# Performance work log

Measured on AMD Instinct MI355X. Metric: run time of the kernel, lower is better.

Reference implementation:

```python
import jax, jax.numpy as jnp
import numpy as np

N = 100_000      # nodes
E = 3_200_000    # edges (avg degree 32)
HID = 64         # hid_dim == in_dim
T = 4            # S2V propagation rounds


def setup_inputs() -> dict:
    key = jax.random.key(0)
    ks = jax.random.split(key, 10)
    s = lambda fan: 1.0 / np.sqrt(fan)
    return {
        "x": jax.random.normal(ks[0], (N, HID), jnp.float32),
        "x_tag": jax.random.uniform(ks[1], (N,), jnp.float32),
        "edge_attr": jax.random.uniform(ks[2], (E, 1), jnp.float32),
        "edge_index": jax.random.randint(ks[3], (2, E), 0, N, dtype=jnp.int32),
        # per-layer bias-free Linear weights (stored as [in, out])
        "W1": jax.random.normal(ks[4], (T, HID), jnp.float32),            # lin1: 1 -> hid
        "W2": jax.random.normal(ks[5], (T, HID, HID), jnp.float32) * s(HID),  # lin2: in -> hid
        "W4": jax.random.normal(ks[6], (T, HID), jnp.float32),            # lin4: 1 -> hid
        "W5": jax.random.normal(ks[7], (2 * HID, 1), jnp.float32) * s(2 * HID),  # lin5
        "W6": jax.random.normal(ks[8], (HID, HID), jnp.float32) * s(HID),  # lin6
        "W7": jax.random.normal(ks[9], (HID, HID), jnp.float32) * s(HID),  # lin7
    }


def reference(x, x_tag, edge_attr, edge_index, W1, W2, W4, W5, W6, W7):
    src = edge_index[0]  # j (message source / p3 scatter target)
    dst = edge_index[1]  # i (aggregation target)
    for l in range(T):  # fixed small layer count
        p1 = x_tag[:, None] * W1[l][None, :]                        # lin1(x_tag)  [N,HID]
        e = jax.nn.relu(edge_attr * W4[l][None, :])                  # relu(lin4(edge_attr)) [E,HID]
        aggr = jax.ops.segment_sum(x[src], dst, num_segments=N)     # add-aggregate x_j at i
        p2 = aggr @ W2[l]                                            # lin2(aggr_out)
        p3 = jax.ops.segment_sum(e, src, num_segments=N)             # scatter_add at edge_index[0]
        x = jax.nn.relu(p1 + p2 + p3)
    graph_pool = jnp.sum(x, axis=0, keepdims=True) @ W6              # [1,HID]
    nodes_vec = x @ W7                                               # [N,HID]
    cat = jnp.concatenate(
        [jnp.broadcast_to(graph_pool, (x.shape[0], graph_pool.shape[1])), nodes_vec], axis=1
    )
    Q = jax.nn.relu(cat) @ W5                                        # [N,1]
    return Q
```

## Files before the change

kernel.cpp:

```cpp
#include <hip/hip_runtime.h>

constexpr int NN  = 100000;
constexpr int NE  = 3200000;
constexpr int HID = 64;
constexpr int TL  = 4;

constexpr int BIN_SHIFT = 9;
constexpr int BIN_NODES = 1 << BIN_SHIFT;
constexpr int NBINS     = (NN + BIN_NODES - 1) / BIN_NODES;
constexpr int BINCAP    = 18944;
constexpr int TILE_E    = 2048;

typedef unsigned short ushort_t;
typedef unsigned int uint_t;
typedef __attribute__((ext_vector_type(8))) short bf16x8;
typedef __attribute__((ext_vector_type(4))) float f32x4;

__device__ __forceinline__ ushort_t f2b(float f) {
  uint_t u = __float_as_uint(f);
  u += 0x7fff + ((u >> 16) & 1);
  return (ushort_t)(u >> 16);
}
__device__ __forceinline__ float b2f(ushort_t h) {
  return __uint_as_float(((uint_t)h) << 16);
}

__global__ __launch_bounds__(256) void escatter_kernel(
    const int* __restrict__ ei, const float* __restrict__ ea,
    int* __restrict__ bincursor, uint_t* __restrict__ gbin,
    int* __restrict__ bincursor2, uint_t* __restrict__ gbin2) {
  __shared__ int hist1[NBINS], base1[NBINS];
  __shared__ int hist2[NBINS], base2[NBINS];
  int tid = threadIdx.x;
  int ntiles = (NE + TILE_E - 1) / TILE_E;
  for (int tile = blockIdx.x; tile < ntiles; tile += gridDim.x) {
    int tb = tile * TILE_E;
    for (int i = tid; i < NBINS; i += 256) { hist1[i] = 0; hist2[i] = 0; }
    __syncthreads();
    uint_t rec1[8], rec2[8]; int bn1[8], bn2[8], rk1[8], rk2[8];
    #pragma unroll
    for (int j = 0; j < 8; ++j) {
      int e = tb + tid + j * 256;
      bn1[j] = -1; bn2[j] = -1;
      rk1[j] = 0; rk2[j] = 0; rec1[j] = 0; rec2[j] = 0;
      if (e < NE) {
        int s = ei[e];
        int d = ei[NE + e];
        uint_t q = (uint_t)(int)(ea[e] * 8388608.0f);
        bn1[j] = d >> BIN_SHIFT;
        rec1[j] = ((uint_t)s << BIN_SHIFT) | (uint_t)(d & (BIN_NODES - 1));
        rk1[j] = atomicAdd(&hist1[bn1[j]], 1);
        bn2[j] = s >> BIN_SHIFT;
        rec2[j] = (q << BIN_SHIFT) | (uint_t)(s & (BIN_NODES - 1));
        rk2[j] = atomicAdd(&hist2[bn2[j]], 1);
      }
    }
    __syncthreads();
    for (int i = tid; i < NBINS; i += 256) {
      int c1 = hist1[i];
      base1[i] = c1 ? atomicAdd(&bincursor[i], c1) : 0;
      int c2 = hist2[i];
      base2[i] = c2 ? atomicAdd(&bincursor2[i], c2) : 0;
    }
    __syncthreads();
    #pragma unroll
    for (int j = 0; j < 8; ++j) {
      if (bn1[j] >= 0) {
        int p1 = base1[bn1[j]] + rk1[j];
        if (p1 < BINCAP) gbin[(size_t)bn1[j] * BINCAP + p1] = rec1[j];
        int p2 = base2[bn2[j]] + rk2[j];
        if (p2 < BINCAP) gbin2[(size_t)bn2[j] * BINCAP + p2] = rec2[j];
      }
    }
    __syncthreads();
  }
}

__global__ __launch_bounds__(256) void binscatter_kernel(
    const int* __restrict__ ei, int* __restrict__ bincursor,
    uint_t* __restrict__ gbin) {
  __shared__ int hist[NBINS];
  __shared__ int base[NBINS];
  int tid = threadIdx.x;
  int ntiles = (NE + TILE_E - 1) / TILE_E;
  for (int tile = blockIdx.x; tile < ntiles; tile += gridDim.x) {
    int tb = tile * TILE_E;
    for (int i = tid; i < NBINS; i += 256) hist[i] = 0;
    __syncthreads();
    uint_t rec[8]; int bn[8]; int rk[8];
    #pragma unroll
    for (int j = 0; j < 8; ++j) {
      int e = tb + tid + j * 256;
      bn[j] = -1; rk[j] = 0; rec[j] = 0;
      if (e < NE) {
        int s = ei[e];
        int d = ei[NE + e];
        bn[j] = d >> BIN_SHIFT;
        rec[j] = ((uint_t)s << BIN_SHIFT) | (uint_t)(d & (BIN_NODES - 1));
        rk[j] = atomicAdd(&hist[bn[j]], 1);
      }
    }
    __syncthreads();
    for (int i = tid; i < NBINS; i += 256) {
      int c = hist[i];
      base[i] = c ? atomicAdd(&bincursor[i], c) : 0;
    }
    __syncthreads();
    #pragma unroll
    for (int j = 0; j < 8; ++j) {
      if (bn[j] >= 0) {
        int pos = base[bn[j]] + rk[j];
        if (pos < BINCAP) gbin[(size_t)bn[j] * BINCAP + pos] = rec[j];
      }
    }
    __syncthreads();
  }
}

__global__ __launch_bounds__(256) void sbinscatter_kernel(
    const int* __restrict__ ei, const float* __restrict__ ea,
    int* __restrict__ bincursor2, uint_t* __restrict__ gbin) {
  __shared__ int hist[NBINS];
  __shared__ int base[NBINS];
  int tid = threadIdx.x;
  int ntiles = (NE + TILE_E - 1) / TILE_E;
  for (int tile = blockIdx.x; tile < ntiles; tile += gridDim.x) {
    int tb = tile * TILE_E;
    for (int i = tid; i < NBINS; i += 256) hist[i] = 0;
    __syncthreads();
    uint_t rec[8]; int bn[8]; int rk[8];
    #pragma unroll
    for (int j = 0; j < 8; ++j) {
      int e = tb + tid + j * 256;
      bn[j] = -1; rk[j] = 0; rec[j] = 0;
      if (e < NE) {
        int s = ei[e];
        uint_t q = (uint_t)(int)(ea[e] * 8388608.0f);
        bn[j] = s >> BIN_SHIFT;
        rec[j] = (q << BIN_SHIFT) | (uint_t)(s & (BIN_NODES - 1));
        rk[j] = atomicAdd(&hist[bn[j]], 1);
      }
    }
    __syncthreads();
    for (int i = tid; i < NBINS; i += 256) {
      int c = hist[i];
      base[i] = c ? atomicAdd(&bincursor2[i], c) : 0;
    }
    __syncthreads();
    #pragma unroll
    for (int j = 0; j < 8; ++j) {
      if (bn[j] >= 0) {
        int pos = base[bn[j]] + rk[j];
        if (pos < BINCAP) gbin[(size_t)bn[j] * BINCAP + pos] = rec[j];
      }
    }
    __syncthreads();
  }
}

__global__ __launch_bounds__(256) void bucket_kernel(
    const uint_t* __restrict__ gbin, const int* __restrict__ bincursor,
    int* __restrict__ colidx, int* __restrict__ cnt, int cap) {
  __shared__ int cur[BIN_NODES];
  int b = blockIdx.x;
  int tid = threadIdx.x;
  for (int i = tid; i < BIN_NODES; i += 256) cur[i] = 0;
  __syncthreads();
  int cb = min(bincursor[b], BINCAP);
  const uint_t* g = gbin + (size_t)b * BINCAP;
  for (int i = tid; i < cb; i += 256) {
    uint_t r = g[i];
    int dl = (int)(r & (BIN_NODES - 1));
    int src = (int)(r >> BIN_SHIFT);
    int pos = atomicAdd(&cur[dl], 1);
    int n = (b << BIN_SHIFT) + dl;
    if (pos < cap) colidx[(size_t)n * cap + pos] = src;
  }
  __syncthreads();
  for (int i = tid; i < BIN_NODES; i += 256) {
    int n = (b << BIN_SHIFT) + i;
    if (n < NN) cnt[n] = min(cur[i], cap);
  }
  for (int gsl = tid; gsl < BIN_NODES * 64; gsl += 256) {
    int i = gsl >> 6;
    int s = gsl & 63;
    int n = (b << BIN_SHIFT) + i;
    if (n < NN && s < 48 && s >= cur[i]) colidx[(size_t)n * cap + s] = NN;
  }
}

__global__ __launch_bounds__(256) void s3bucket_kernel(
    const uint_t* __restrict__ gbin, const int* __restrict__ bincursor2,
    int* __restrict__ s3i) {
  __shared__ int acc[BIN_NODES];
  int b = blockIdx.x;
  int tid = threadIdx.x;
  for (int i = tid; i < BIN_NODES; i += 256) acc[i] = 0;
  __syncthreads();
  int cb = min(bincursor2[b], BINCAP);
  const uint_t* g = gbin + (size_t)b * BINCAP;
  for (int i = tid; i < cb; i += 256) {
    uint_t r = g[i];
    atomicAdd(&acc[r & (BIN_NODES - 1)], (int)(r >> BIN_SHIFT));
  }
  __syncthreads();
  for (int i = tid; i < BIN_NODES; i += 256) {
    int n = (b << BIN_SHIFT) + i;
    if (n < NN) s3i[n] = acc[i];
  }
}

__global__ void conv_kernel(const float* __restrict__ x, ushort_t* __restrict__ xb) {
  int i = blockIdx.x * blockDim.x + threadIdx.x;
  if (i * 4 >= NN * HID) return;
  const float4 v = *reinterpret_cast<const float4*>(&x[i * 4]);
  ushort4 o;
  o.x = f2b(v.x); o.y = f2b(v.y); o.z = f2b(v.z); o.w = f2b(v.w);
  *reinterpret_cast<ushort4*>(&xb[i * 4]) = o;
}

__global__ void wconv_kernel(const float* __restrict__ W2,
                             const float* __restrict__ W7,
                             ushort_t* __restrict__ w2t,
                             ushort_t* __restrict__ w7t) {
  int i = blockIdx.x * blockDim.x + threadIdx.x;
  int tot2 = TL * HID * HID;
  if (i < tot2) {
    int l = i >> 12, r = i & 4095, h = r >> 6, k = r & 63;
    w2t[i] = f2b(W2[(size_t)l * 4096 + k * 64 + h]);
  } else if (i < tot2 + HID * HID) {
    int j = i - tot2, h = j >> 6, k = j & 63;
    w7t[j] = f2b(W7[k * 64 + h]);
  }
}

__global__ __launch_bounds__(256) void dense_kernel(
    const ushort_t* __restrict__ xin, const ushort_t* __restrict__ wt,
    ushort_t* __restrict__ yout) {
  int lane = threadIdx.x & 63;
  int wv = (blockIdx.x * blockDim.x + threadIdx.x) >> 6;
  int n0 = wv * 32;
  if (n0 >= NN) return;
  int row = lane & 15;
  int ks = (lane >> 4) * 8;
  bf16x8 a0 = *(const bf16x8*)&xin[(size_t)(n0 + row) * HID + ks];
  bf16x8 a1 = *(const bf16x8*)&xin[(size_t)(n0 + row) * HID + 32 + ks];
  bf16x8 a2 = *(const bf16x8*)&xin[(size_t)(n0 + 16 + row) * HID + ks];
  bf16x8 a3 = *(const bf16x8*)&xin[(size_t)(n0 + 16 + row) * HID + 32 + ks];
  #pragma unroll
  for (int ct = 0; ct < 4; ++ct) {
    bf16x8 b0 = *(const bf16x8*)&wt[(ct * 16 + row) * HID + ks];
    bf16x8 b1 = *(const bf16x8*)&wt[(ct * 16 + row) * HID + 32 + ks];
    f32x4 acc0 = {0.f, 0.f, 0.f, 0.f};
    f32x4 acc1 = {0.f, 0.f, 0.f, 0.f};
    acc0 = __builtin_amdgcn_mfma_f32_16x16x32_bf16(a0, b0, acc0, 0, 0, 0);
    acc0 = __builtin_amdgcn_mfma_f32_16x16x32_bf16(a1, b1, acc0, 0, 0, 0);
    acc1 = __builtin_amdgcn_mfma_f32_16x16x32_bf16(a2, b0, acc1, 0, 0, 0);
    acc1 = __builtin_amdgcn_mfma_f32_16x16x32_bf16(a3, b1, acc1, 0, 0, 0);
    int rr = (lane >> 4) * 4;
    #pragma unroll
    for (int r = 0; r < 4; ++r) {
      yout[(size_t)(n0 + rr + r) * HID + ct * 16 + row] = f2b(acc0[r]);
      yout[(size_t)(n0 + 16 + rr + r) * HID + ct * 16 + row] = f2b(acc1[r]);
    }
  }
}

__global__ __launch_bounds__(256) void aggr_kernel(
    const ushort_t* __restrict__ yin, ushort_t* __restrict__ xout,
    const int* __restrict__ cnt, const int* __restrict__ colidx, int cap,
    const float* __restrict__ x_tag, const int* __restrict__ s3i,
    const float* __restrict__ W1l, const float* __restrict__ W4l) {
  int lane = threadIdx.x & 63;
  int wv = (blockIdx.x * blockDim.x + threadIdx.x) >> 6;
  int n0 = wv * 2;
  if (n0 >= NN) return;
  int half = lane >> 5;
  int n = n0 + half;
  int grp = (lane >> 3) & 3;
  int sub = lane & 7;
  const int* cl = colidx + (size_t)n * cap + grp;
  float f0 = 0.f, f1 = 0.f, f2 = 0.f, f3 = 0.f;
  float f4 = 0.f, f5 = 0.f, f6 = 0.f, f7 = 0.f;
  uint4 w[12];
  #pragma unroll
  for (int j = 0; j < 12; ++j) {
    int c = cl[j * 4];
    w[j] = *reinterpret_cast<const uint4*>(&yin[(size_t)c * HID + sub * 8]);
  }
  #pragma unroll
  for (int j = 0; j < 12; ++j) {
    f0 += __uint_as_float(w[j].x << 16);
    f1 += __uint_as_float(w[j].x & 0xffff0000u);
    f2 += __uint_as_float(w[j].y << 16);
    f3 += __uint_as_float(w[j].y & 0xffff0000u);
    f4 += __uint_as_float(w[j].z << 16);
    f5 += __uint_as_float(w[j].z & 0xffff0000u);
    f6 += __uint_as_float(w[j].w << 16);
    f7 += __uint_as_float(w[j].w & 0xffff0000u);
  }
  int deg = cnt[n];
  if (__any(deg > 48)) {
    int t2 = deg - 48;
    const int* ct2 = colidx + (size_t)n * cap + 48;
    for (int jt = 0; jt < 12; ++jt) {
      int idx = jt * 4 + grp;
      if (idx < t2) {
        int c = ct2[idx];
        uint4 ww = *reinterpret_cast<const uint4*>(&yin[(size_t)c * HID + sub * 8]);
        f0 += __uint_as_float(ww.x << 16);
        f1 += __uint_as_float(ww.x & 0xffff0000u);
        f2 += __uint_as_float(ww.y << 16);
        f3 += __uint_as_float(ww.y & 0xffff0000u);
        f4 += __uint_as_float(ww.z << 16);
        f5 += __uint_as_float(ww.z & 0xffff0000u);
        f6 += __uint_as_float(ww.w << 16);
        f7 += __uint_as_float(ww.w & 0xffff0000u);
      }
    }
  }
  #pragma unroll
  for (int m = 8; m <= 16; m <<= 1) {
    f0 += __shfl_xor(f0, m); f1 += __shfl_xor(f1, m);
    f2 += __shfl_xor(f2, m); f3 += __shfl_xor(f3, m);
    f4 += __shfl_xor(f4, m); f5 += __shfl_xor(f5, m);
    f6 += __shfl_xor(f6, m); f7 += __shfl_xor(f7, m);
  }
  float xt = x_tag[n];
  float s3f = (float)s3i[n] * 0x1p-23f;
  float4 w1a = *reinterpret_cast<const float4*>(&W1l[sub * 8]);
  float4 w1b = *reinterpret_cast<const float4*>(&W1l[sub * 8 + 4]);
  float4 w4a = *reinterpret_cast<const float4*>(&W4l[sub * 8]);
  float4 w4b = *reinterpret_cast<const float4*>(&W4l[sub * 8 + 4]);
  float o0 = fmaxf(fmaf(xt, w1a.x, fmaf(s3f, fmaxf(w4a.x, 0.f), f0)), 0.f);
  float o1 = fmaxf(fmaf(xt, w1a.y, fmaf(s3f, fmaxf(w4a.y, 0.f), f1)), 0.f);
  float o2 = fmaxf(fmaf(xt, w1a.z, fmaf(s3f, fmaxf(w4a.z, 0.f), f2)), 0.f);
  float o3 = fmaxf(fmaf(xt, w1a.w, fmaf(s3f, fmaxf(w4a.w, 0.f), f3)), 0.f);
  float o4 = fmaxf(fmaf(xt, w1b.x, fmaf(s3f, fmaxf(w4b.x, 0.f), f4)), 0.f);
  float o5 = fmaxf(fmaf(xt, w1b.y, fmaf(s3f, fmaxf(w4b.y, 0.f), f5)), 0.f);
  float o6 = fmaxf(fmaf(xt, w1b.z, fmaf(s3f, fmaxf(w4b.z, 0.f), f6)), 0.f);
  float o7 = fmaxf(fmaf(xt, w1b.w, fmaf(s3f, fmaxf(w4b.w, 0.f), f7)), 0.f);
  if (grp == 0) {
    uint4 o;
    o.x = (uint_t)f2b(o0) | ((uint_t)f2b(o1) << 16);
    o.y = (uint_t)f2b(o2) | ((uint_t)f2b(o3) << 16);
    o.z = (uint_t)f2b(o4) | ((uint_t)f2b(o5) << 16);
    o.w = (uint_t)f2b(o6) | ((uint_t)f2b(o7) << 16);
    *reinterpret_cast<uint4*>(&xout[(size_t)n * HID + sub * 8]) = o;
  }
}

__global__ __launch_bounds__(256) void qdense_kernel(
    const ushort_t* __restrict__ xin, const ushort_t* __restrict__ w7t,
    const float* __restrict__ w5hi, float* __restrict__ Qr,
    float* __restrict__ sumx) {
  __shared__ float ssum[4][HID];
  int tid = threadIdx.x;
  int lane = tid & 63;
  int wloc = tid >> 6;
  int wv = (blockIdx.x * blockDim.x + tid) >> 6;
  int n0 = wv * 16;
  bool valid = n0 < NN;
  int n0c = valid ? n0 : 0;
  int row = lane & 15;
  int g = lane >> 4;
  int ks = g * 8;
  bf16x8 a0 = *(const bf16x8*)&xin[(size_t)(n0c + row) * HID + ks];
  bf16x8 a1 = *(const bf16x8*)&xin[(size_t)(n0c + row) * HID + 32 + ks];
  float r0 = 0.f, r1 = 0.f, r2 = 0.f, r3 = 0.f;
  #pragma unroll
  for (int ct = 0; ct < 4; ++ct) {
    bf16x8 b0 = *(const bf16x8*)&w7t[(ct * 16 + row) * HID + ks];
    bf16x8 b1 = *(const bf16x8*)&w7t[(ct * 16 + row) * HID + 32 + ks];
    f32x4 acc = {0.f, 0.f, 0.f, 0.f};
    acc = __builtin_amdgcn_mfma_f32_16x16x32_bf16(a0, b0, acc, 0, 0, 0);
    acc = __builtin_amdgcn_mfma_f32_16x16x32_bf16(a1, b1, acc, 0, 0, 0);
    float w5 = w5hi[ct * 16 + row];
    r0 += fmaxf(acc[0], 0.f) * w5;
    r1 += fmaxf(acc[1], 0.f) * w5;
    r2 += fmaxf(acc[2], 0.f) * w5;
    r3 += fmaxf(acc[3], 0.f) * w5;
  }
  #pragma unroll
  for (int m = 1; m <= 8; m <<= 1) {
    r0 += __shfl_xor(r0, m); r1 += __shfl_xor(r1, m);
    r2 += __shfl_xor(r2, m); r3 += __shfl_xor(r3, m);
  }
  if (valid && row == 0) {
    int rb = n0 + g * 4;
    Qr[rb + 0] = r0; Qr[rb + 1] = r1; Qr[rb + 2] = r2; Qr[rb + 3] = r3;
  }
  float c[16];
  #pragma unroll
  for (int e = 0; e < 8; ++e) {
    c[e]     = valid ? b2f((ushort_t)a0[e]) : 0.f;
    c[8 + e] = valid ? b2f((ushort_t)a1[e]) : 0.f;
  }
  #pragma unroll
  for (int m = 1; m <= 8; m <<= 1) {
    #pragma unroll
    for (int e = 0; e < 16; ++e) c[e] += __shfl_xor(c[e], m);
  }
  if (row == 0) {
    #pragma unroll
    for (int e = 0; e < 8; ++e) {
      ssum[wloc][ks + e] = c[e];
      ssum[wloc][32 + ks + e] = c[8 + e];
    }
  }
  __syncthreads();
  if (tid < HID) {
    float s = ssum[0][tid] + ssum[1][tid] + ssum[2][tid] + ssum[3][tid];
    atomicAdd(&sumx[tid], s);
  }
}

__global__ void pool_kernel(const float* __restrict__ sumx, const float* __restrict__ W6,
                            const float* __restrict__ W5, float* __restrict__ c0) {
  int lane = threadIdx.x & 63;
  float sv = sumx[lane];
  float gp = 0.f;
  #pragma unroll
  for (int k = 0; k < HID; ++k) {
    float a = __int_as_float(__builtin_amdgcn_readlane(__float_as_int(sv), k));
    gp = fmaf(a, W6[k * HID + lane], gp);
  }
  float r = fmaxf(gp, 0.f) * W5[lane];
  #pragma unroll
  for (int m = 32; m >= 1; m >>= 1) r += __shfl_xor(r, m);
  if (lane == 0) *c0 = r;
}

__global__ void qfix_kernel(float* __restrict__ Q, const float* __restrict__ c0) {
  int i = blockIdx.x * blockDim.x + threadIdx.x;
  if (i < NN) Q[i] += *c0;
}

extern "C" void kernel_launch(void* const* d_in, const int* in_sizes, int n_in,
                              void* d_out, int out_size, void* d_ws, size_t ws_size,
                              hipStream_t stream) {
  const float* x         = (const float*)d_in[0];
  const float* x_tag     = (const float*)d_in[1];
  const float* edge_attr = (const float*)d_in[2];
  const int*   edge_index= (const int*)d_in[3];
  const float* W1        = (const float*)d_in[4];
  const float* W2        = (const float*)d_in[5];
  const float* W4        = (const float*)d_in[6];
  const float* W5        = (const float*)d_in[7];
  const float* W6        = (const float*)d_in[8];
  const float* W7        = (const float*)d_in[9];
  float* Q = (float*)d_out;

  const int QBLOCKS = ((NN / 16) * 64 + 255) / 256;

  char* ws = (char*)d_ws;
  size_t off = 0;
  auto alloc = [&](size_t bytes) -> void* {
    void* p = ws + off;
    off = (off + bytes + 255) & ~(size_t)255;
    return p;
  };
  int*      bincursor  = (int*)alloc(NBINS * 4);
  int*      bincursor2 = (int*)alloc(NBINS * 4);
  float*    sumx       = (float*)alloc(HID * 4);
  size_t zero_bytes = off;
  int*      s3i    = (int*)alloc(NN * 4);
  int*      cnt    = (int*)alloc(NN * 4);
  float*    c0     = (float*)alloc(4);
  ushort_t* xb0    = (ushort_t*)alloc((size_t)NN * HID * 2);
  ushort_t* xb1    = (ushort_t*)alloc((size_t)NN * HID * 2);
  ushort_t* ybuf   = (ushort_t*)alloc((size_t)(NN + 1) * HID * 2);
  ushort_t* w2t    = (ushort_t*)alloc((size_t)TL * HID * HID * 2);
  ushort_t* w7t    = (ushort_t*)alloc((size_t)HID * HID * 2);
  uint_t*   gbin   = (uint_t*)alloc((size_t)NBINS * BINCAP * 4);

  size_t off_nog2 = off;
  uint_t* gbin2 = (uint_t*)alloc((size_t)NBINS * BINCAP * 4);
  bool merged = true;
  {
    size_t rem = (ws_size > off) ? (ws_size - off) : 0;
    if ((int)(rem / ((size_t)NN * 4)) < 64) { merged = false; off = off_nog2; }
  }
  size_t rem = (ws_size > off) ? (ws_size - off) : 0;
  int cap = (int)(rem / ((size_t)NN * 4));
  if (cap > 96) cap = 96;
  if (cap < 64) cap = 64;
  int* colidx = (int*)alloc((size_t)NN * cap * 4);

  hipMemsetAsync(d_ws, 0, zero_bytes, stream);
  hipMemsetAsync(ybuf + (size_t)NN * HID, 0, HID * 2, stream);

  if (merged) {
    escatter_kernel<<<512, 256, 0, stream>>>(edge_index, edge_attr,
                                             bincursor, gbin, bincursor2, gbin2);
    bucket_kernel<<<NBINS, 256, 0, stream>>>(gbin, bincursor, colidx, cnt, cap);
    s3bucket_kernel<<<NBINS, 256, 0, stream>>>(gbin2, bincursor2, s3i);
  } else {
    binscatter_kernel<<<512, 256, 0, stream>>>(edge_index, bincursor, gbin);
    bucket_kernel<<<NBINS, 256, 0, stream>>>(gbin, bincursor, colidx, cnt, cap);
    sbinscatter_kernel<<<512, 256, 0, stream>>>(edge_index, edge_attr, bincursor2, gbin);
    s3bucket_kernel<<<NBINS, 256, 0, stream>>>(gbin, bincursor2, s3i);
  }
  conv_kernel<<<(NN * HID / 4 + 255) / 256, 256, 0, stream>>>(x, xb0);
  wconv_kernel<<<((TL + 1) * HID * HID + 255) / 256, 256, 0, stream>>>(W2, W7, w2t, w7t);

  int ablocks = ((NN / 2) * 64 + 255) / 256;
  int dblocks = ((NN / 32) * 64 + 255) / 256;
  const ushort_t* xi = xb0;
  ushort_t* xo = xb1;
  for (int l = 0; l < TL; ++l) {
    dense_kernel<<<dblocks, 256, 0, stream>>>(xi, w2t + (size_t)l * HID * HID, ybuf);
    aggr_kernel<<<ablocks, 256, 0, stream>>>(ybuf, xo, cnt, colidx, cap,
                                             x_tag, s3i, W1 + l * HID, W4 + l * HID);
    ushort_t* tmp = (ushort_t*)xi;
    xi = xo;
    xo = (l == 0) ? xb0 : tmp;
  }

  qdense_kernel<<<QBLOCKS, 256, 0, stream>>>(xi, w7t, W5 + HID, Q, sumx);
  pool_kernel<<<1, 64, 0, stream>>>(sumx, W6, W5, c0);
  qfix_kernel<<<(NN + 255) / 256, 256, 0, stream>>>(Q, c0);
}
```

Baseline: 426.3 us.

## Stage binned edge records in shared memory for coalesced global writes

The merged edge-binning kernel now does a block-wide prefix scan over its per-bin histogram and reorders each tile's records in LDS by bin. It then writes them to the global bins in contiguous runs rather than as scattered per-thread stores. The persistent grid-stride loop is replaced by one block per tile, and the binscatter kernels' launch sizes change to match. This trades extra LDS traffic and barriers for better-coalesced global writes.

```diff
diff --git a/kernel.cpp b/kernel.cpp
--- a/kernel.cpp
+++ b/kernel.cpp
@@ -29,50 +29,79 @@
     const int* __restrict__ ei, const float* __restrict__ ea,
     int* __restrict__ bincursor, uint_t* __restrict__ gbin,
     int* __restrict__ bincursor2, uint_t* __restrict__ gbin2) {
-  __shared__ int hist1[NBINS], base1[NBINS];
-  __shared__ int hist2[NBINS], base2[NBINS];
+  __shared__ int hist1[256], hist2[256];
+  __shared__ int base1[NBINS], base2[NBINS];
+  __shared__ int offs1[NBINS], offs2[NBINS];
+  __shared__ uint_t srec[TILE_E];
+  __shared__ int    sdst[TILE_E];
   int tid = threadIdx.x;
-  int ntiles = (NE + TILE_E - 1) / TILE_E;
-  for (int tile = blockIdx.x; tile < ntiles; tile += gridDim.x) {
-    int tb = tile * TILE_E;
-    for (int i = tid; i < NBINS; i += 256) { hist1[i] = 0; hist2[i] = 0; }
-    __syncthreads();
-    uint_t rec1[8], rec2[8]; int bn1[8], bn2[8], rk1[8], rk2[8];
-    #pragma unroll
-    for (int j = 0; j < 8; ++j) {
-      int e = tb + tid + j * 256;
-      bn1[j] = -1; bn2[j] = -1;
-      rk1[j] = 0; rk2[j] = 0; rec1[j] = 0; rec2[j] = 0;
-      if (e < NE) {
-        int s = ei[e];
-        int d = ei[NE + e];
-        uint_t q = (uint_t)(int)(ea[e] * 8388608.0f);
-        bn1[j] = d >> BIN_SHIFT;
-        rec1[j] = ((uint_t)s << BIN_SHIFT) | (uint_t)(d & (BIN_NODES - 1));
-        rk1[j] = atomicAdd(&hist1[bn1[j]], 1);
-        bn2[j] = s >> BIN_SHIFT;
-        rec2[j] = (q << BIN_SHIFT) | (uint_t)(s & (BIN_NODES - 1));
-        rk2[j] = atomicAdd(&hist2[bn2[j]], 1);
-      }
-    }
-    __syncthreads();
-    for (int i = tid; i < NBINS; i += 256) {
-      int c1 = hist1[i];
-      base1[i] = c1 ? atomicAdd(&bincursor[i], c1) : 0;
-      int c2 = hist2[i];
-      base2[i] = c2 ? atomicAdd(&bincursor2[i], c2) : 0;
-    }
-    __syncthreads();
-    #pragma unroll
-    for (int j = 0; j < 8; ++j) {
-      if (bn1[j] >= 0) {
-        int p1 = base1[bn1[j]] + rk1[j];
-        if (p1 < BINCAP) gbin[(size_t)bn1[j] * BINCAP + p1] = rec1[j];
-        int p2 = base2[bn2[j]] + rk2[j];
-        if (p2 < BINCAP) gbin2[(size_t)bn2[j] * BINCAP + p2] = rec2[j];
-      }
-    }
-    __syncthreads();
+  int tb = blockIdx.x * TILE_E;
+  hist1[tid] = 0; hist2[tid] = 0;
+  __syncthreads();
+  uint_t rec1[8], rec2[8]; int bn1[8], bn2[8], rk1[8], rk2[8];
+  #pragma unroll
+  for (int j = 0; j < 8; ++j) {
+    int e = tb + tid + j * 256;
+    bn1[j] = -1; bn2[j] = -1;
+    rk1[j] = 0; rk2[j] = 0; rec1[j] = 0; rec2[j] = 0;
+    if (e < NE) {
+      int s = ei[e];
+      int d = ei[NE + e];
+      uint_t q = (uint_t)(int)(ea[e] * 8388608.0f);
+      bn1[j] = d >> BIN_SHIFT;
+      rec1[j] = ((uint_t)s << BIN_SHIFT) | (uint_t)(d & (BIN_NODES - 1));
+      rk1[j] = atomicAdd(&hist1[bn1[j]], 1);
+      bn2[j] = s >> BIN_SHIFT;
+      rec2[j] = (q << BIN_SHIFT) | (uint_t)(s & (BIN_NODES - 1));
+      rk2[j] = atomicAdd(&hist2[bn2[j]], 1);
+    }
+  }
+  __syncthreads();
+  int c1 = hist1[tid], c2 = hist2[tid];
+  for (int o = 1; o < 256; o <<= 1) {
+    int a1 = (tid >= o) ? hist1[tid - o] : 0;
+    int a2 = (tid >= o) ? hist2[tid - o] : 0;
+    __syncthreads();
+    hist1[tid] += a1; hist2[tid] += a2;
+    __syncthreads();
+  }
+  if (tid < NBINS) {
+    offs1[tid] = hist1[tid] - c1;
+    offs2[tid] = hist2[tid] - c2;
+    base1[tid] = c1 ? atomicAdd(&bincursor[tid], c1) : 0;
+    base2[tid] = c2 ? atomicAdd(&bincursor2[tid], c2) : 0;
+  }
+  __syncthreads();
+  int total1 = hist1[NBINS - 1];
+  int total2 = hist2[NBINS - 1];
+  #pragma unroll
+  for (int j = 0; j < 8; ++j) {
+    if (bn1[j] >= 0) {
+      int p = offs1[bn1[j]] + rk1[j];
+      int gp = base1[bn1[j]] + rk1[j];
+      srec[p] = rec1[j];
+      sdst[p] = (gp < BINCAP) ? (bn1[j] * BINCAP + gp) : -1;
+    }
+  }
+  __syncthreads();
+  for (int t = tid; t < total1; t += 256) {
+    int g = sdst[t];
+    if (g >= 0) gbin[g] = srec[t];
+  }
+  __syncthreads();
+  #pragma unroll
+  for (int j = 0; j < 8; ++j) {
+    if (bn2[j] >= 0) {
+      int p = offs2[bn2[j]] + rk2[j];
+      int gp = base2[bn2[j]] + rk2[j];
+      srec[p] = rec2[j];
+      sdst[p] = (gp < BINCAP) ? (bn2[j] * BINCAP + gp) : -1;
+    }
+  }
+  __syncthreads();
+  for (int t = tid; t < total2; t += 256) {
+    int g = sdst[t];
+    if (g >= 0) gbin2[g] = srec[t];
   }
 }
 
@@ -452,6 +481,7 @@
   float* Q = (float*)d_out;
 
   const int QBLOCKS = ((NN / 16) * 64 + 255) / 256;
+  const int NTILES  = (NE + TILE_E - 1) / TILE_E;
 
   char* ws = (char*)d_ws;
   size_t off = 0;
@@ -491,14 +521,14 @@
   hipMemsetAsync(ybuf + (size_t)NN * HID, 0, HID * 2, stream);
 
   if (merged) {
-    escatter_kernel<<<512, 256, 0, stream>>>(edge_index, edge_attr,
-                                             bincursor, gbin, bincursor2, gbin2);
+    escatter_kernel<<<NTILES, 256, 0, stream>>>(edge_index, edge_attr,
+                                                bincursor, gbin, bincursor2, gbin2);
     bucket_kernel<<<NBINS, 256, 0, stream>>>(gbin, bincursor, colidx, cnt, cap);
     s3bucket_kernel<<<NBINS, 256, 0, stream>>>(gbin2, bincursor2, s3i);
   } else {
-    binscatter_kernel<<<512, 256, 0, stream>>>(edge_index, bincursor, gbin);
+    binscatter_kernel<<<NTILES, 256, 0, stream>>>(edge_index, bincursor, gbin);
     bucket_kernel<<<NBINS, 256, 0, stream>>>(gbin, bincursor, colidx, cnt, cap);
-    sbinscatter_kernel<<<512, 256, 0, stream>>>(edge_index, edge_attr, bincursor2, gbin);
+    sbinscatter_kernel<<<NTILES, 256, 0, stream>>>(edge_index, edge_attr, bincursor2, gbin);
     s3bucket_kernel<<<NBINS, 256, 0, stream>>>(gbin, bincursor2, s3i);
   }
   conv_kernel<<<(NN * HID / 4 + 255) / 256, 256, 0, stream>>>(x, xb0);
```

Measured after the change: 430.6 us. No clear change (+1.0%).
